# Kernel tuning notes

Hardware: AMD Instinct MI355X
Metric: run time of the kernel (lower is better)

Reference implementation:

```python
import jax, jax.numpy as jnp
import numpy as np

N_NODES = 100000
N_EDGES = 1600000
IN_DIM, HID, LAT = 128, 64, 64
NEG_SLOPE = 0.2


def gat_layer(x, W, att_src, att_dst, bias, src, dst, n_nodes):
    # PyG GATConv, heads=1: linear transform, edge attention logits,
    # per-destination segment softmax, weighted scatter-sum, bias.
    h = x @ W                              # [N, D]
    a_s = h @ att_src                      # [N]
    a_d = h @ att_dst                      # [N]
    e = a_s[src] + a_d[dst]                # [E]
    e = jnp.where(e > 0, e, NEG_SLOPE * e)  # leaky_relu
    m = jax.ops.segment_max(e, dst, num_segments=n_nodes)
    ex = jnp.exp(e - m[dst])
    denom = jax.ops.segment_sum(ex, dst, num_segments=n_nodes)
    alpha = ex / denom[dst]                # [E]
    out = jax.ops.segment_sum(alpha[:, None] * h[src], dst, num_segments=n_nodes)
    return out + bias


def setup_inputs() -> dict:
    key = jax.random.key(0)
    ks = jax.random.split(key, 12)
    x = jax.random.normal(ks[0], (N_NODES, IN_DIM), dtype=jnp.float32)
    edge_index = jax.random.randint(ks[1], (2, N_EDGES), 0, N_NODES, dtype=jnp.int64 if jax.config.jax_enable_x64 else jnp.int32)
    edge_attr = jax.random.normal(ks[2], (N_EDGES, 8), dtype=jnp.float32)
    def glorot(k, shape):
        fan = shape[0] + shape[-1]
        return jax.random.uniform(k, shape, jnp.float32, -1.0, 1.0) * np.sqrt(6.0 / fan)
    W1 = glorot(ks[3], (IN_DIM, HID))
    att_src1 = glorot(ks[4], (HID,))
    att_dst1 = glorot(ks[5], (HID,))
    b1 = jnp.zeros((HID,), jnp.float32)
    W2 = glorot(ks[6], (HID, LAT))
    att_src2 = glorot(ks[7], (LAT,))
    att_dst2 = glorot(ks[8], (LAT,))
    b2 = jnp.zeros((LAT,), jnp.float32)
    Wl = glorot(ks[9], (LAT, LAT))
    bl = jnp.zeros((LAT,), jnp.float32)
    return {"x": x, "edge_index": edge_index, "edge_attr": edge_attr,
            "W1": W1, "att_src1": att_src1, "att_dst1": att_dst1, "b1": b1,
            "W2": W2, "att_src2": att_src2, "att_dst2": att_dst2, "b2": b2,
            "Wl": Wl, "bl": bl}


def reference(x, edge_index, edge_attr, W1, att_src1, att_dst1, b1,
              W2, att_src2, att_dst2, b2, Wl, bl):
    n = x.shape[0]
    # add_self_loops=True (PyG default); edge_attr unused (edge_dim=None)
    loops = jnp.arange(n, dtype=edge_index.dtype)
    src = jnp.concatenate([edge_index[0], loops])
    dst = jnp.concatenate([edge_index[1], loops])
    h = gat_layer(x, W1, att_src1, att_dst1, b1, src, dst, n)
    h = jax.nn.relu(h)  # dropout inactive in eval mode
    h = gat_layer(h, W2, att_src2, att_dst2, b2, src, dst, n)
    return h @ Wl + bl
```

## Files before the change

kernel.cpp:

```cpp
#include <hip/hip_runtime.h>
#include <hip/hip_bf16.h>
#include <math.h>

#define BS_LOG 9
#define BS (1 << BS_LOG)
#define NBMAX 256
#define CHUNK 8192


__global__ __launch_bounds__(256) void bucket_hist(const int* __restrict__ ei, int E, int tot,
                                                   int* __restrict__ ghist) {
    __shared__ int h[NBMAX];
    int t = threadIdx.x;
    h[t] = 0;
    __syncthreads();
    int lo = blockIdx.x * CHUNK, hi = min(lo + CHUNK, tot);
    for (int i = lo + t; i < hi; i += 256) {
        int d = (i < E) ? ei[E + i] : (i - E);
        atomicAdd(&h[d >> BS_LOG], 1);
    }
    __syncthreads();
    if (h[t]) atomicAdd(&ghist[t], h[t]);
}

__global__ __launch_bounds__(256) void bucket_scan(const int* __restrict__ ghist, int nb, int tot,
                                                   int* __restrict__ bkt_ptr, int* __restrict__ gcursor,
                                                   int* __restrict__ row_ptr, int n) {
    __shared__ int sh[256];
    int t = threadIdx.x;
    int v = (t < nb) ? ghist[t] : 0;
    sh[t] = v;
    __syncthreads();
    for (int off = 1; off < 256; off <<= 1) {
        int u = (t >= off) ? sh[t - off] : 0;
        __syncthreads();
        sh[t] += u;
        __syncthreads();
    }
    int excl = sh[t] - v;
    bkt_ptr[t] = excl;
    gcursor[t] = excl;
    if (t == 0) row_ptr[n] = tot;
}

__global__ __launch_bounds__(256) void partition_k(const int* __restrict__ ei, int E, int tot,
                                                   int* __restrict__ gcursor, int2* __restrict__ ebuf) {
    __shared__ int h[NBMAX];
    __shared__ int base_s[NBMAX];
    int t = threadIdx.x;
    h[t] = 0;
    __syncthreads();
    int lo = blockIdx.x * CHUNK, hi = min(lo + CHUNK, tot);
    for (int i = lo + t; i < hi; i += 256) {
        int d = (i < E) ? ei[E + i] : (i - E);
        atomicAdd(&h[d >> BS_LOG], 1);
    }
    __syncthreads();
    int c = h[t];
    if (c) base_s[t] = atomicAdd(&gcursor[t], c);
    __syncthreads();
    h[t] = 0;
    __syncthreads();
    for (int i = lo + t; i < hi; i += 256) {
        int s, d;
        if (i < E) { s = ei[i]; d = ei[E + i]; } else { s = i - E; d = s; }
        int b = d >> BS_LOG;
        int pos = base_s[b] + atomicAdd(&h[b], 1);
        ebuf[pos] = make_int2(s, d);
    }
}

__global__ __launch_bounds__(256) void bucket_csr(const int2* __restrict__ ebuf,
                                                  const int* __restrict__ bkt_ptr, int n,
                                                  int* __restrict__ row_ptr, int* __restrict__ csr_src) {
    __shared__ int cnt[BS];
    __shared__ int ssum[256];
    int t = threadIdx.x;
    int lo = blockIdx.x << BS_LOG;
    int ebeg = bkt_ptr[blockIdx.x], eend = bkt_ptr[blockIdx.x + 1];
    cnt[t] = 0; cnt[t + 256] = 0;
    __syncthreads();
    for (int i = ebeg + t; i < eend; i += 256)
        atomicAdd(&cnt[ebuf[i].y - lo], 1);
    __syncthreads();
    int a0 = cnt[2 * t], a1 = cnt[2 * t + 1];
    ssum[t] = a0 + a1;
    __syncthreads();
    for (int off = 1; off < 256; off <<= 1) {
        int u = (t >= off) ? ssum[t - off] : 0;
        __syncthreads();
        ssum[t] += u;
        __syncthreads();
    }
    int ex = t ? ssum[t - 1] : 0;
    cnt[2 * t] = ex;
    cnt[2 * t + 1] = ex + a0;
    int d0 = lo + 2 * t;
    if (d0 < n)     row_ptr[d0]     = ebeg + ex;
    if (d0 + 1 < n) row_ptr[d0 + 1] = ebeg + ex + a0;
    __syncthreads();
    for (int i = ebeg + t; i < eend; i += 256) {
        int2 e = ebuf[i];
        int pos = ebeg + atomicAdd(&cnt[e.y - lo], 1);
        csr_src[pos] = e.x;
    }
}


template<int K, bool ATT, bool BIAS>
__global__ __launch_bounds__(256) void gemm_att(
    const float* __restrict__ X, const float* __restrict__ W,
    const float* __restrict__ attS, const float* __restrict__ attD,
    const float* __restrict__ bias,
    float* __restrict__ H, float* __restrict__ aS, float* __restrict__ aD, int n) {
    __shared__ float4 Wt4[(K / 4) * 64];
    __shared__ float attl[128];
    __shared__ float bl_[64];
    int tid = threadIdx.x;
    for (int i = tid; i < (K / 4) * 64; i += 256) {
        int k = (i >> 6) * 4, c = i & 63;
        Wt4[i] = make_float4(W[(k + 0) * 64 + c], W[(k + 1) * 64 + c],
                             W[(k + 2) * 64 + c], W[(k + 3) * 64 + c]);
    }
    if (ATT && tid < 64) { attl[tid] = attS[tid]; attl[64 + tid] = attD[tid]; }
    if (BIAS && tid < 64) bl_[tid] = bias[tid];
    __syncthreads();

    int c = tid & 63;
    int wv = __builtin_amdgcn_readfirstlane(tid >> 6);
    int base = blockIdx.x * 16;
    int row0 = base + wv * 4;
    int rr0 = min(row0 + 0, n - 1), rr1 = min(row0 + 1, n - 1);
    int rr2 = min(row0 + 2, n - 1), rr3 = min(row0 + 3, n - 1);
    const float4* x0 = reinterpret_cast<const float4*>(X + (size_t)rr0 * K);
    const float4* x1 = reinterpret_cast<const float4*>(X + (size_t)rr1 * K);
    const float4* x2 = reinterpret_cast<const float4*>(X + (size_t)rr2 * K);
    const float4* x3 = reinterpret_cast<const float4*>(X + (size_t)rr3 * K);

    float a0 = 0.f, a1 = 0.f, a2 = 0.f, a3 = 0.f;
    #pragma unroll 4
    for (int k4 = 0; k4 < K / 4; ++k4) {
        float4 w = Wt4[k4 * 64 + c];
        float4 p0 = x0[k4];
        float4 p1 = x1[k4];
        float4 p2 = x2[k4];
        float4 p3 = x3[k4];
        a0 += w.x * p0.x + w.y * p0.y + w.z * p0.z + w.w * p0.w;
        a1 += w.x * p1.x + w.y * p1.y + w.z * p1.z + w.w * p1.w;
        a2 += w.x * p2.x + w.y * p2.y + w.z * p2.z + w.w * p2.w;
        a3 += w.x * p3.x + w.y * p3.y + w.z * p3.z + w.w * p3.w;
    }
    float accs[4] = {a0, a1, a2, a3};
    #pragma unroll
    for (int j = 0; j < 4; ++j) {
        int node = row0 + j;
        if (node >= n) break;
        float v = accs[j];
        if (BIAS) v += bl_[c];
        H[(size_t)node * 64 + c] = v;
        if (ATT) {
            float vs = accs[j] * attl[c];
            float vd = accs[j] * attl[64 + c];
            for (int off = 32; off > 0; off >>= 1) {
                vs += __shfl_xor(vs, off, 64);
                vd += __shfl_xor(vd, off, 64);
            }
            if (c == 0) { aS[node] = vs; aD[node] = vd; }
        }
    }
}


template<bool RELU>
__global__ __launch_bounds__(256) void aggregate(
    const float* __restrict__ H, const float* __restrict__ aS, const float* __restrict__ aD,
    const float* __restrict__ bias, const int* __restrict__ row_ptr,
    const int* __restrict__ csr_src, float* __restrict__ out, int n) {
    int lane = threadIdx.x & 63;
    int node = blockIdx.x * 4 + (threadIdx.x >> 6);
    if (node >= n) return;
    int start = row_ptr[node], end = row_ptr[node + 1];
    int deg = end - start;
    float adv = aD[node];
    int fl = lane & 15, slot = lane >> 4;
    float4 acc = {0.f, 0.f, 0.f, 0.f};

    if (deg <= 64) {
        bool valid = lane < deg;
        int s_mine = csr_src[valid ? (start + lane) : start];
        float e = aS[s_mine] + adv;
        e = e > 0.f ? e : 0.2f * e;
        float m = valid ? e : -1e30f;
        #pragma unroll
        for (int off = 1; off < 64; off <<= 1) m = fmaxf(m, __shfl_xor(m, off, 64));
        float ex = valid ? __expf(e - m) : 0.f;
        float d = ex;
        #pragma unroll
        for (int off = 1; off < 64; off <<= 1) d += __shfl_xor(d, off, 64);
        float p_mine = ex * (1.0f / d);

        for (int j0 = 0; j0 < deg; j0 += 8) {
            int ja = j0 + slot, jb = j0 + 4 + slot;
            float pa = __shfl(p_mine, ja, 64);
            float pb = __shfl(p_mine, jb, 64);
            int sa = __shfl(s_mine, ja, 64);
            int sb = __shfl(s_mine, jb, 64);
            if (ja >= deg) pa = 0.f;
            if (jb >= deg) pb = 0.f;
            float4 va = *(reinterpret_cast<const float4*>(H + (size_t)sa * 64) + fl);
            float4 vb = *(reinterpret_cast<const float4*>(H + (size_t)sb * 64) + fl);
            acc.x += pa * va.x + pb * vb.x;
            acc.y += pa * va.y + pb * vb.y;
            acc.z += pa * va.z + pb * vb.z;
            acc.w += pa * va.w + pb * vb.w;
        }
    } else {
        float m = -1e30f, d = 0.f;
        for (int idx = start + lane; idx < end; idx += 64) {
            int s = csr_src[idx];
            float e = aS[s] + adv;
            e = e > 0.f ? e : 0.2f * e;
            if (e > m) { d *= __expf(m - e); m = e; }
            d += __expf(e - m);
        }
        #pragma unroll
        for (int off = 1; off < 64; off <<= 1) {
            float m2 = __shfl_xor(m, off, 64);
            float d2 = __shfl_xor(d, off, 64);
            float mn = fmaxf(m, m2);
            d = d * __expf(m - mn) + d2 * __expf(m2 - mn);
            m = mn;
        }
        float invd = 1.0f / d;
        for (int j0 = 0; j0 < deg; j0 += 4) {
            int j = j0 + slot;
            bool v = j < deg;
            int s = csr_src[v ? (start + j) : start];
            float e = aS[s] + adv;
            e = e > 0.f ? e : 0.2f * e;
            float p = v ? __expf(e - m) * invd : 0.f;
            float4 hv = *(reinterpret_cast<const float4*>(H + (size_t)s * 64) + fl);
            acc.x += p * hv.x;
            acc.y += p * hv.y;
            acc.z += p * hv.z;
            acc.w += p * hv.w;
        }
    }

    #pragma unroll
    for (int off = 16; off <= 32; off <<= 1) {
        acc.x += __shfl_xor(acc.x, off, 64);
        acc.y += __shfl_xor(acc.y, off, 64);
        acc.z += __shfl_xor(acc.z, off, 64);
        acc.w += __shfl_xor(acc.w, off, 64);
    }
    if (lane < 16) {
        float4 b4 = reinterpret_cast<const float4*>(bias)[fl];
        acc.x += b4.x; acc.y += b4.y; acc.z += b4.z; acc.w += b4.w;
        if (RELU) {
            acc.x = fmaxf(acc.x, 0.f);
            acc.y = fmaxf(acc.y, 0.f);
            acc.z = fmaxf(acc.z, 0.f);
            acc.w = fmaxf(acc.w, 0.f);
        }
        reinterpret_cast<float4*>(out + (size_t)node * 64)[fl] = acc;
    }
}


extern "C" void kernel_launch(void* const* d_in, const int* in_sizes, int n_in,
                              void* d_out, int out_size, void* d_ws, size_t ws_size,
                              hipStream_t stream) {
    const float* x   = (const float*)d_in[0];
    const int*   ei  = (const int*)  d_in[1];
    const float* W1  = (const float*)d_in[3];
    const float* as1 = (const float*)d_in[4];
    const float* ad1 = (const float*)d_in[5];
    const float* b1  = (const float*)d_in[6];
    const float* W2  = (const float*)d_in[7];
    const float* as2 = (const float*)d_in[8];
    const float* ad2 = (const float*)d_in[9];
    const float* b2  = (const float*)d_in[10];
    const float* Wlw = (const float*)d_in[11];
    const float* blw = (const float*)d_in[12];

    int n = in_sizes[0] / 128;
    int E = in_sizes[1] / 2;
    int tot = E + n;
    int NB = (n + BS - 1) >> BS_LOG;

    char* ws = (char*)d_ws;
    size_t off = 0;
    auto alloc = [&](size_t bytes) {
        void* p = ws + off;
        off = (off + bytes + 255) & ~(size_t)255;
        return p;
    };
    int*   ghist   = (int*)  alloc(NBMAX * 4);
    int*   bkt_ptr = (int*)  alloc((NBMAX + 1) * 4);
    int*   gcursor = (int*)  alloc(NBMAX * 4);
    int*   row_ptr = (int*)  alloc((size_t)(n + 1) * 4);
    int*   csr_src = (int*)  alloc((size_t)tot * 4);
    float* h1      = (float*)alloc((size_t)n * 64 * 4);
    float* hr      = (float*)alloc((size_t)n * 64 * 4);
    float* aS      = (float*)alloc((size_t)n * 4);
    float* aD      = (float*)alloc((size_t)n * 4);
    int2*  ebuf    = (int2*)h1;

    hipMemsetAsync(ghist, 0, NBMAX * 4, stream);
    int NBLK = (tot + CHUNK - 1) / CHUNK;
    bucket_hist<<<NBLK, 256, 0, stream>>>(ei, E, tot, ghist);
    bucket_scan<<<1, 256, 0, stream>>>(ghist, NB, tot, bkt_ptr, gcursor, row_ptr, n);
    partition_k<<<NBLK, 256, 0, stream>>>(ei, E, tot, gcursor, ebuf);
    bucket_csr<<<NB, 256, 0, stream>>>(ebuf, bkt_ptr, n, row_ptr, csr_src);

    int gb = (n + 15) / 16;
    int ab = (n + 3) / 4;

    gemm_att<128, true, false><<<gb, 256, 0, stream>>>(x, W1, as1, ad1, nullptr, h1, aS, aD, n);
    aggregate<true><<<ab, 256, 0, stream>>>(h1, aS, aD, b1, row_ptr, csr_src, hr, n);

    gemm_att<64, true, false><<<gb, 256, 0, stream>>>(hr, W2, as2, ad2, nullptr, h1, aS, aD, n);
    aggregate<false><<<ab, 256, 0, stream>>>(h1, aS, aD, b2, row_ptr, csr_src, hr, n);

    gemm_att<64, false, true><<<gb, 256, 0, stream>>>(hr, Wlw, nullptr, nullptr, blw,
                                                      (float*)d_out, nullptr, nullptr, n);
}
```

Baseline: 488.8 us.

## Tile GEMM with shared-memory X staging and 4x4 register blocking

Rewrites the dense transform kernel so each block stages a 64-row tile of X into padded shared memory and each thread computes a 4-row by 4-column register tile, instead of one column for four rows read straight from global memory. W is copied into LDS in its natural layout. The attention-dot reductions now shuffle across 16 lanes rather than 64. This is meant to raise arithmetic intensity and cut redundant global loads of X. In exchange LDS use per block grows (about 40KB for K=128), which may lower occupancy.

```diff
diff --git a/kernel.cpp b/kernel.cpp
--- a/kernel.cpp
+++ b/kernel.cpp
@@ -113,59 +113,72 @@
     const float* __restrict__ attS, const float* __restrict__ attD,
     const float* __restrict__ bias,
     float* __restrict__ H, float* __restrict__ aS, float* __restrict__ aD, int n) {
-    __shared__ float4 Wt4[(K / 4) * 64];
+    constexpr int K4 = K / 4;
+    constexpr int XSS = K4 + 1;
+    __shared__ float4 xs4[64 * XSS];
+    __shared__ float4 Ws4[K * 16];
     __shared__ float attl[128];
     __shared__ float bl_[64];
     int tid = threadIdx.x;
-    for (int i = tid; i < (K / 4) * 64; i += 256) {
-        int k = (i >> 6) * 4, c = i & 63;
-        Wt4[i] = make_float4(W[(k + 0) * 64 + c], W[(k + 1) * 64 + c],
-                             W[(k + 2) * 64 + c], W[(k + 3) * 64 + c]);
-    }
+
+    const float4* W4 = reinterpret_cast<const float4*>(W);
+    for (int i = tid; i < K * 16; i += 256) Ws4[i] = W4[i];
     if (ATT && tid < 64) { attl[tid] = attS[tid]; attl[64 + tid] = attD[tid]; }
     if (BIAS && tid < 64) bl_[tid] = bias[tid];
-    __syncthreads();
-
-    int c = tid & 63;
-    int wv = __builtin_amdgcn_readfirstlane(tid >> 6);
-    int base = blockIdx.x * 16;
-    int row0 = base + wv * 4;
-    int rr0 = min(row0 + 0, n - 1), rr1 = min(row0 + 1, n - 1);
-    int rr2 = min(row0 + 2, n - 1), rr3 = min(row0 + 3, n - 1);
-    const float4* x0 = reinterpret_cast<const float4*>(X + (size_t)rr0 * K);
-    const float4* x1 = reinterpret_cast<const float4*>(X + (size_t)rr1 * K);
-    const float4* x2 = reinterpret_cast<const float4*>(X + (size_t)rr2 * K);
-    const float4* x3 = reinterpret_cast<const float4*>(X + (size_t)rr3 * K);
-
-    float a0 = 0.f, a1 = 0.f, a2 = 0.f, a3 = 0.f;
-    #pragma unroll 4
-    for (int k4 = 0; k4 < K / 4; ++k4) {
-        float4 w = Wt4[k4 * 64 + c];
-        float4 p0 = x0[k4];
-        float4 p1 = x1[k4];
-        float4 p2 = x2[k4];
-        float4 p3 = x3[k4];
-        a0 += w.x * p0.x + w.y * p0.y + w.z * p0.z + w.w * p0.w;
-        a1 += w.x * p1.x + w.y * p1.y + w.z * p1.z + w.w * p1.w;
-        a2 += w.x * p2.x + w.y * p2.y + w.z * p2.z + w.w * p2.w;
-        a3 += w.x * p3.x + w.y * p3.y + w.z * p3.z + w.w * p3.w;
-    }
-    float accs[4] = {a0, a1, a2, a3};
+
+    int base = blockIdx.x * 64;
+    const float4* X4 = reinterpret_cast<const float4*>(X);
+    for (int i = tid; i < 64 * K4; i += 256) {
+        int r = i / K4, k4 = i % K4;
+        int gr = base + r;
+        xs4[r * XSS + k4] = (gr < n) ? X4[(size_t)gr * K4 + k4]
+                                     : make_float4(0.f, 0.f, 0.f, 0.f);
+    }
+    __syncthreads();
+
+    int lane = tid & 63, w = tid >> 6;
+    int cl = lane & 15;
+    int rg = lane >> 4;
+    int c0 = cl * 4;
+    int row_local = w * 16 + rg * 4;
+
+    float acc[4][4] = {};
+    #pragma unroll 2
+    for (int k4 = 0; k4 < K4; ++k4) {
+        float4 wv0 = Ws4[(k4 * 4 + 0) * 16 + cl];
+        float4 wv1 = Ws4[(k4 * 4 + 1) * 16 + cl];
+        float4 wv2 = Ws4[(k4 * 4 + 2) * 16 + cl];
+        float4 wv3 = Ws4[(k4 * 4 + 3) * 16 + cl];
+        #pragma unroll
+        for (int j = 0; j < 4; ++j) {
+            float4 xv = xs4[(row_local + j) * XSS + k4];
+            acc[j][0] += xv.x * wv0.x + xv.y * wv1.x + xv.z * wv2.x + xv.w * wv3.x;
+            acc[j][1] += xv.x * wv0.y + xv.y * wv1.y + xv.z * wv2.y + xv.w * wv3.y;
+            acc[j][2] += xv.x * wv0.z + xv.y * wv1.z + xv.z * wv2.z + xv.w * wv3.z;
+            acc[j][3] += xv.x * wv0.w + xv.y * wv1.w + xv.z * wv2.w + xv.w * wv3.w;
+        }
+    }
+
     #pragma unroll
     for (int j = 0; j < 4; ++j) {
-        int node = row0 + j;
-        if (node >= n) break;
-        float v = accs[j];
-        if (BIAS) v += bl_[c];
-        H[(size_t)node * 64 + c] = v;
+        int node = base + row_local + j;
+        bool live = node < n;
+        float4 o;
+        o.x = acc[j][0]; o.y = acc[j][1]; o.z = acc[j][2]; o.w = acc[j][3];
+        if (BIAS) { o.x += bl_[c0]; o.y += bl_[c0 + 1]; o.z += bl_[c0 + 2]; o.w += bl_[c0 + 3]; }
+        if (live)
+            *reinterpret_cast<float4*>(H + (size_t)node * 64 + c0) = o;
         if (ATT) {
-            float vs = accs[j] * attl[c];
-            float vd = accs[j] * attl[64 + c];
-            for (int off = 32; off > 0; off >>= 1) {
-                vs += __shfl_xor(vs, off, 64);
-                vd += __shfl_xor(vd, off, 64);
+            float ps = acc[j][0] * attl[c0]      + acc[j][1] * attl[c0 + 1]
+                     + acc[j][2] * attl[c0 + 2]  + acc[j][3] * attl[c0 + 3];
+            float pd = acc[j][0] * attl[64 + c0]     + acc[j][1] * attl[64 + c0 + 1]
+                     + acc[j][2] * attl[64 + c0 + 2] + acc[j][3] * attl[64 + c0 + 3];
+            #pragma unroll
+            for (int off = 1; off <= 8; off <<= 1) {
+                ps += __shfl_xor(ps, off, 64);
+                pd += __shfl_xor(pd, off, 64);
             }
-            if (c == 0) { aS[node] = vs; aD[node] = vd; }
+            if (live && cl == 0) { aS[node] = ps; aD[node] = pd; }
         }
     }
 }
@@ -314,7 +327,7 @@
     partition_k<<<NBLK, 256, 0, stream>>>(ei, E, tot, gcursor, ebuf);
     bucket_csr<<<NB, 256, 0, stream>>>(ebuf, bkt_ptr, n, row_ptr, csr_src);
 
-    int gb = (n + 15) / 16;
+    int gb = (n + 63) / 64;
     int ab = (n + 3) / 4;
 
     gemm_att<128, true, false><<<gb, 256, 0, stream>>>(x, W1, as1, ad1, nullptr, h1, aS, aD, n);
```

Measured after the change: 432.2 us. 1.13x faster.
